# Kernel tuning notes

Measured on AMD Instinct MI355X. Metric: run time of the kernel, lower is better.

The kernel has to match this reference:

```python
import jax, jax.numpy as jnp
import numpy as np

EMBED = 1024
HEADS = 16
HEAD_DIM = EMBED // HEADS


def setup_inputs() -> dict:
    key = jax.random.key(0)
    ks = jax.random.split(key, 11)
    B, S, D = 4, 2048, EMBED
    scale = 1.0 / np.sqrt(D)
    inp = {
        "query": jax.random.normal(ks[0], (B, S, D), dtype=jnp.float32),
        "key": jax.random.normal(ks[1], (B, S, D), dtype=jnp.float32),
        "value": jax.random.normal(ks[2], (B, S, D), dtype=jnp.float32),
        "Wq": jax.random.normal(ks[3], (D, D), dtype=jnp.float32) * scale,
        "bq": jnp.zeros((D,), dtype=jnp.float32),
        "Wk": jax.random.normal(ks[4], (D, D), dtype=jnp.float32) * scale,
        "bk": jnp.zeros((D,), dtype=jnp.float32),
        "Wv": jax.random.normal(ks[5], (D, D), dtype=jnp.float32) * scale,
        "bv": jnp.zeros((D,), dtype=jnp.float32),
        "Wo": jax.random.normal(ks[6], (D, D), dtype=jnp.float32) * scale,
        "bo": jnp.zeros((D,), dtype=jnp.float32),
    }
    return inp


def reference(query, key, value, Wq, bq, Wk, bk, Wv, bv, Wo, bo):
    B, S, D = query.shape
    H, Hd = HEADS, HEAD_DIM

    def split_heads(x):  # [B,S,D] -> [B,H,S,Hd]
        return x.reshape(B, -1, H, Hd).transpose(0, 2, 1, 3)

    q = split_heads(query @ Wq.T + bq)
    k = split_heads(key @ Wk.T + bk)
    v = split_heads(value @ Wv.T + bv)
    # [B,H,S,S] scores (explicitly materialized, as in the original)
    attn = jnp.einsum("bhsd,bhtd->bhst", q, k) / jnp.sqrt(jnp.float32(Hd))
    attn = jax.nn.softmax(attn, axis=-1)  # dropout p=0.0 is identity
    out = jnp.einsum("bhst,bhtd->bhsd", attn, v)
    out = out.transpose(0, 2, 1, 3).reshape(B, -1, D)
    return out @ Wo.T + bo
```

## Files before the change

kernel.cpp:

```cpp
#include <hip/hip_runtime.h>
#include <stdint.h>

typedef __bf16 bf16x8_t __attribute__((ext_vector_type(8)));
typedef float f32x2_t __attribute__((ext_vector_type(2)));
typedef float f32x4_t __attribute__((ext_vector_type(4)));
typedef float f32x8_t __attribute__((ext_vector_type(8)));
typedef float f32x16_t __attribute__((ext_vector_type(16)));
typedef uint16_t u16x8_t __attribute__((ext_vector_type(8)));
typedef uint16_t u16x4_t __attribute__((ext_vector_type(4)));
typedef uint32_t u32x4_t __attribute__((ext_vector_type(4)));

#define MFMA16(a, b, c) __builtin_amdgcn_mfma_f32_16x16x32_bf16((a), (b), (c), 0, 0, 0)
#define MFMA32(a, b, c) __builtin_amdgcn_mfma_f32_32x32x16_bf16((a), (b), (c), 0, 0, 0)

__device__ __forceinline__ void gll16(const void* g, void* l) {
  typedef const __attribute__((address_space(1))) void* gp1_t;
  typedef __attribute__((address_space(3))) void* lp3_t;
  __builtin_amdgcn_global_load_lds((gp1_t)(uintptr_t)g,
                                   (lp3_t)(uint32_t)(uintptr_t)l, 16, 0, 0);
}

__device__ __forceinline__ uint16_t f2bf(float f) {
  uint32_t u = __float_as_uint(f);
  u += 0x7fffu + ((u >> 16) & 1u);
  return (uint16_t)(u >> 16);
}

__device__ __forceinline__ uint32_t cvtpk(float lo, float hi) {
  uint32_t r;
  asm("v_cvt_pk_bf16_f32 %0, %1, %2" : "=v"(r) : "v"(lo), "v"(hi));
  return r;
}

__device__ __forceinline__ void pl32swap(uint32_t& x, uint32_t& y) {
  asm("v_permlane32_swap_b32 %0, %1" : "+v"(x), "+v"(y));
}

__device__ __forceinline__ float fexp2(float x) {
#if __has_builtin(__builtin_amdgcn_exp2f)
  return __builtin_amdgcn_exp2f(x);
#else
  return exp2f(x);
#endif
}

__global__ __launch_bounds__(256) void cvt_all_kernel(
    const float* __restrict__ q, const float* __restrict__ k, const float* __restrict__ v,
    const float* __restrict__ wq, const float* __restrict__ wk, const float* __restrict__ wv,
    const float* __restrict__ wo, uint16_t* __restrict__ oq, uint16_t* __restrict__ ok,
    uint16_t* __restrict__ ov, uint16_t* __restrict__ owq, uint16_t* __restrict__ owk,
    uint16_t* __restrict__ owv, uint16_t* __restrict__ owo, float qscale) {
  const int bid = blockIdx.x;
  const float* in;
  uint16_t* out;
  int i;
  float sc = 1.0f;
  if (bid < 12288) {
    const int seg = bid >> 12;
    in = seg == 0 ? q : (seg == 1 ? k : v);
    out = seg == 0 ? oq : (seg == 1 ? ok : ov);
    i = (bid & 4095) * 256 + threadIdx.x;
  } else {
    const int wb = bid - 12288, seg = wb >> 9;
    in = seg == 0 ? wq : (seg == 1 ? wk : (seg == 2 ? wv : wo));
    out = seg == 0 ? owq : (seg == 1 ? owk : (seg == 2 ? owv : owo));
    if (seg == 0) sc = qscale;
    i = (wb & 511) * 256 + threadIdx.x;
  }
  const float4* p = (const float4*)in;
  float4 a = p[2 * i], b = p[2 * i + 1];
  u16x8_t o;
  o[0] = f2bf(a.x * sc); o[1] = f2bf(a.y * sc);
  o[2] = f2bf(a.z * sc); o[3] = f2bf(a.w * sc);
  o[4] = f2bf(b.x * sc); o[5] = f2bf(b.y * sc);
  o[6] = f2bf(b.z * sc); o[7] = f2bf(b.w * sc);
  ((u16x8_t*)out)[i] = o;
}

#define GEMM_KLOOP(Ab, Bb)                                                                   \
  _Pragma("unroll") for (int s = 0; s < 4; ++s) {                                            \
    const int rbase = s * 32 + w * 8;                                                        \
    gll16(Ab + (size_t)(bm0 + rbase + srow) * (K * 2) + scb, AsB + rbase * 128);             \
    gll16(Bb + (size_t)(bn0 + rbase + srow) * (K * 2) + scb, BsB + rbase * 128);             \
  }                                                                                          \
  for (int it = 0; it < K / 64; ++it) {                                                      \
    const int cur = (it & 1) * 16384;                                                        \
    asm volatile("s_waitcnt vmcnt(0)\ns_barrier" ::: "memory");                              \
    if (it < 15) {                                                                           \
      const int k0 = (it + 1) * 64;                                                          \
      const int nxt = (cur ^ 16384);                                                         \
      _Pragma("unroll") for (int s = 0; s < 4; ++s) {                                        \
        const int rbase = s * 32 + w * 8;                                                    \
        gll16(Ab + (size_t)(bm0 + rbase + srow) * (K * 2) + k0 * 2 + scb,                    \
              AsB + nxt + rbase * 128);                                                      \
        gll16(Bb + (size_t)(bn0 + rbase + srow) * (K * 2) + k0 * 2 + scb,                    \
              BsB + nxt + rbase * 128);                                                      \
      }                                                                                      \
    }                                                                                        \
    _Pragma("unroll") for (int kk = 0; kk < 2; ++kk) {                                       \
      bf16x8_t af[4], bfr[4];                                                                \
      _Pragma("unroll") for (int f = 0; f < 4; ++f) {                                        \
        const int ar = wr * 64 + f * 16 + lrow;                                              \
        af[f] =                                                                              \
            *(const bf16x8_t*)(AsB + cur + ar * 128 + ((kk * 64 + g * 16) ^ ((ar & 7) << 4)));\
        const int br = wc * 64 + f * 16 + lrow;                                              \
        bfr[f] =                                                                             \
            *(const bf16x8_t*)(BsB + cur + br * 128 + ((kk * 64 + g * 16) ^ ((br & 7) << 4)));\
      }                                                                                      \
      __builtin_amdgcn_s_setprio(1);                                                         \
      _Pragma("unroll") for (int fm = 0; fm < 4; ++fm) _Pragma("unroll")                     \
          for (int fn = 0; fn < 4; ++fn) acc[fm][fn] = MFMA16(af[fm], bfr[fn], acc[fm][fn]); \
      __builtin_amdgcn_s_setprio(0);                                                         \
    }                                                                                        \
  }

__global__ __launch_bounds__(256) void gemm_qkv_kernel(
    const uint16_t* __restrict__ Xq, const uint16_t* __restrict__ Xk,
    const uint16_t* __restrict__ Xv, const uint16_t* __restrict__ Wqb,
    const uint16_t* __restrict__ Wkb, const uint16_t* __restrict__ Wvb,
    const float* __restrict__ bq, const float* __restrict__ bk, const float* __restrict__ bv,
    uint16_t* __restrict__ Qp, uint16_t* __restrict__ Kp, uint16_t* __restrict__ VTp,
    float qscale) {
  constexpr int K = 1024, N = 1024;
  __shared__ uint16_t As[2][128 * 64];
  __shared__ uint16_t Bs[2][128 * 64];
  char* AsB = (char*)As;
  char* BsB = (char*)Bs;
  const int tid = threadIdx.x;
  const int w = tid >> 6, l = tid & 63;
  const int wr = w >> 1, wc = w & 1;
  const int lrow = l & 15, g = l >> 4;
  const int bm0 = blockIdx.y * 128, bn0 = blockIdx.x * 128;
  const int srow = l >> 3;
  const int scb = ((l & 7) ^ srow) << 4;
  const int z = blockIdx.z;
  const char* Ab = (const char*)(z == 0 ? Xq : (z == 1 ? Xk : Xv));
  const char* Bb = (const char*)(z == 0 ? Wqb : (z == 1 ? Wkb : Wvb));
  const float* bias = z == 0 ? bq : (z == 1 ? bk : bv);
  const float alpha = z == 0 ? qscale : 1.0f;
  f32x4_t acc[4][4] = {};

  GEMM_KLOOP(Ab, Bb)

#pragma unroll
  for (int fn = 0; fn < 4; ++fn) {
    const int col = bn0 + wc * 64 + fn * 16 + lrow;
    const float bv_ = bias[col] * alpha;
#pragma unroll
    for (int fm = 0; fm < 4; ++fm) {
      const int row0 = bm0 + wr * 64 + fm * 16 + g * 4;
      const int b = row0 >> 11, t = row0 & 2047;
      const int bhh = (b << 4) + (col >> 6), d = col & 63;
      if (z == 0) {
#pragma unroll
        for (int r = 0; r < 4; ++r)
          Qp[(size_t)(row0 + r) * N + col] = f2bf(acc[fm][fn][r] + bv_);
      } else if (z == 1) {
#pragma unroll
        for (int r = 0; r < 4; ++r)
          Kp[((size_t)bhh * 2048 + t + r) * 64 + d] = f2bf(acc[fm][fn][r] + bv_);
      } else {
        u16x4_t pv;
#pragma unroll
        for (int r = 0; r < 4; ++r) pv[r] = f2bf(acc[fm][fn][r] + bv_);
        const size_t idx = (((size_t)bhh * 32 + (t >> 6)) * 64 + d) * 64 + (t & 63);
        *(u16x4_t*)(VTp + idx) = pv;
      }
    }
  }
}

__global__ __launch_bounds__(256) void gemm_out_kernel(const uint16_t* __restrict__ A,
                                                       const uint16_t* __restrict__ Bw,
                                                       const float* __restrict__ bias,
                                                       float* __restrict__ C) {
  constexpr int K = 1024, N = 1024;
  __shared__ uint16_t As[2][128 * 64];
  __shared__ uint16_t Bs[2][128 * 64];
  char* AsB = (char*)As;
  char* BsB = (char*)Bs;
  const int tid = threadIdx.x;
  const int w = tid >> 6, l = tid & 63;
  const int wr = w >> 1, wc = w & 1;
  const int lrow = l & 15, g = l >> 4;
  const int bm0 = blockIdx.y * 128, bn0 = blockIdx.x * 128;
  const int srow = l >> 3;
  const int scb = ((l & 7) ^ srow) << 4;
  const char* Ab = (const char*)A;
  const char* Bb = (const char*)Bw;
  f32x4_t acc[4][4] = {};

  GEMM_KLOOP(Ab, Bb)

#pragma unroll
  for (int fn = 0; fn < 4; ++fn) {
    const int col = bn0 + wc * 64 + fn * 16 + lrow;
    const float bv_ = bias[col];
#pragma unroll
    for (int fm = 0; fm < 4; ++fm) {
      const int row0 = bm0 + wr * 64 + fm * 16 + g * 4;
#pragma unroll
      for (int r = 0; r < 4; ++r) C[(size_t)(row0 + r) * N + col] = acc[fm][fn][r] + bv_;
    }
  }
}

__global__ __launch_bounds__(256, 4) void attn_kernel(const uint16_t* __restrict__ Q,
                                                      const uint16_t* __restrict__ Kh,
                                                      const uint16_t* __restrict__ VT,
                                                      uint16_t* __restrict__ AO) {
  constexpr int S = 2048, D = 1024;
  __shared__ uint16_t Kb[2][64 * 64];
  __shared__ uint16_t Vb[2][64 * 64];
  char* KbB = (char*)Kb;
  char* VbB = (char*)Vb;
  const int tid = threadIdx.x;
  const int w = tid >> 6, l = tid & 63;
  const int lr = l & 31, hi = l >> 5;
  const int flat = blockIdx.x;
  const int xcd = flat & 7, ii = flat >> 3;
  const int bh = xcd * 8 + (ii & 7);
  const int qt = ii >> 3;
  const int b = bh >> 4, h = bh & 15;
  const int q0 = qt * 128;
  const int srow = l >> 3;
  const int sofs0 = (w * 8 + srow) * 128 + (((l & 7) ^ srow ^ (w & 3)) << 4);
  const int swz = ((l & 7) ^ ((l >> 3) & 3)) << 4;
  const char* Kg = (const char*)Kh + (size_t)bh * 262144;
  const char* Vg = (const char*)VT + (size_t)bh * 262144;

  const char* qrow =
      (const char*)Q + (size_t)(b * S + q0 + w * 32 + lr) * (D * 2) + h * 128 + hi * 16;
  bf16x8_t qf[4];
#pragma unroll
  for (int km = 0; km < 4; ++km) qf[km] = *(const bf16x8_t*)(qrow + km * 32);

  float l_run = 0.f;
  f32x16_t acco[2] = {};

  gll16(Kg + sofs0, KbB + w * 1024);
  gll16(Kg + 4096 + sofs0, KbB + 4096 + w * 1024);
  gll16(Vg + sofs0, VbB + w * 1024);
  gll16(Vg + 4096 + sofs0, VbB + 4096 + w * 1024);

#pragma unroll 2
  for (int t = 0; t < 32; ++t) {
    const int cur = (t & 1) * 8192;
    asm volatile("s_waitcnt vmcnt(0)\ns_barrier" ::: "memory");

    if (t < 31) {
      const size_t nb = (size_t)(t + 1) * 8192 + sofs0;
      const int nl = (cur ^ 8192) + w * 1024;
      gll16(Kg + nb, KbB + nl);
      gll16(Kg + nb + 4096, KbB + nl + 4096);
      gll16(Vg + nb, VbB + nl);
      gll16(Vg + nb + 4096, VbB + nl + 4096);
    }

    f32x16_t s0 = {}, s1 = {};
    __builtin_amdgcn_s_setprio(1);
#pragma unroll
    for (int km = 0; km < 4; ++km) {
      const int co = (km * 32 + hi * 16) ^ swz;
      bf16x8_t kf0 = *(const bf16x8_t*)(KbB + cur + lr * 128 + co);
      bf16x8_t kf1 = *(const bf16x8_t*)(KbB + cur + (32 + lr) * 128 + co);
      s0 = MFMA32(kf0, qf[km], s0);
      s1 = MFMA32(kf1, qf[km], s1);
    }
    __builtin_amdgcn_s_setprio(0);

#pragma unroll
    for (int j = 0; j < 16; ++j) {
      s0[j] = fexp2(s0[j]);
      s1[j] = fexp2(s1[j]);
    }
    {
      f32x16_t sv = s0 + s1;
      f32x8_t a8 = __builtin_shufflevector(sv, sv, 0, 1, 2, 3, 4, 5, 6, 7) +
                   __builtin_shufflevector(sv, sv, 8, 9, 10, 11, 12, 13, 14, 15);
      f32x4_t a4 = __builtin_shufflevector(a8, a8, 0, 1, 2, 3) +
                   __builtin_shufflevector(a8, a8, 4, 5, 6, 7);
      f32x2_t a2 = __builtin_shufflevector(a4, a4, 0, 1) +
                   __builtin_shufflevector(a4, a4, 2, 3);
      float rs = a2[0] + a2[1];
      rs += __shfl_xor(rs, 32);
      l_run += rs;
    }

    uint32_t cw[16];
#pragma unroll
    for (int j = 0; j < 8; ++j) cw[j] = cvtpk(s0[2 * j], s0[2 * j + 1]);
#pragma unroll
    for (int j = 0; j < 8; ++j) cw[8 + j] = cvtpk(s1[2 * j], s1[2 * j + 1]);
    pl32swap(cw[0], cw[2]);
    pl32swap(cw[1], cw[3]);
    pl32swap(cw[4], cw[6]);
    pl32swap(cw[5], cw[7]);
    pl32swap(cw[8], cw[10]);
    pl32swap(cw[9], cw[11]);
    pl32swap(cw[12], cw[14]);
    pl32swap(cw[13], cw[15]);

    __builtin_amdgcn_s_setprio(1);
#pragma unroll
    for (int kb = 0; kb < 4; ++kb) {
      u32x4_t pwv = {cw[kb * 4], cw[kb * 4 + 1], cw[kb * 4 + 2], cw[kb * 4 + 3]};
      bf16x8_t pa = __builtin_bit_cast(bf16x8_t, pwv);
#pragma unroll
      for (int db = 0; db < 2; ++db) {
        bf16x8_t vf = *(const bf16x8_t*)(VbB + cur + (db * 32 + lr) * 128 +
                                         ((kb * 32 + hi * 16) ^ swz));
        acco[db] = MFMA32(vf, pa, acco[db]);
      }
    }
    __builtin_amdgcn_s_setprio(0);
  }

  const float inv = 1.0f / l_run;
  uint16_t* orow = AO + (size_t)(b * S + q0 + w * 32 + lr) * D + h * 64 + hi * 4;
#pragma unroll
  for (int db = 0; db < 2; ++db)
#pragma unroll
    for (int rr = 0; rr < 4; ++rr) {
      u16x4_t o;
#pragma unroll
      for (int j = 0; j < 4; ++j) o[j] = f2bf(acco[db][rr * 4 + j] * inv);
      *(u16x4_t*)(orow + db * 32 + rr * 8) = o;
    }
}

extern "C" void kernel_launch(void* const* d_in, const int* in_sizes, int n_in,
                              void* d_out, int out_size, void* d_ws, size_t ws_size,
                              hipStream_t stream) {
  const float* q_in = (const float*)d_in[0];
  const float* k_in = (const float*)d_in[1];
  const float* v_in = (const float*)d_in[2];
  const float* Wq = (const float*)d_in[3];
  const float* bq = (const float*)d_in[4];
  const float* Wk = (const float*)d_in[5];
  const float* bk = (const float*)d_in[6];
  const float* Wv = (const float*)d_in[7];
  const float* bv = (const float*)d_in[8];
  const float* Wo = (const float*)d_in[9];
  const float* bo = (const float*)d_in[10];

  const size_t MD = (size_t)8192 * 1024;
  const size_t DD = (size_t)1024 * 1024;
  uint16_t* Xq = (uint16_t*)d_ws;
  uint16_t* Xk = Xq + MD;
  uint16_t* Xv = Xk + MD;
  uint16_t* Wqb = Xv + MD;
  uint16_t* Wkb = Wqb + DD;
  uint16_t* Wvb = Wkb + DD;
  uint16_t* Wob = Wvb + DD;
  uint16_t* Qp = Wob + DD;
  uint16_t* Kp = Qp + MD;
  uint16_t* VTp = Kp + MD;
  uint16_t* AO = Xq;

  const float QSCALE = 0.125f * 1.44269504088896f;

  cvt_all_kernel<<<14336, 256, 0, stream>>>(q_in, k_in, v_in, Wq, Wk, Wv, Wo, Xq, Xk, Xv,
                                            Wqb, Wkb, Wvb, Wob, QSCALE);

  gemm_qkv_kernel<<<dim3(8, 64, 3), 256, 0, stream>>>(Xq, Xk, Xv, Wqb, Wkb, Wvb, bq, bk, bv,
                                                      Qp, Kp, VTp, QSCALE);

  attn_kernel<<<1024, 256, 0, stream>>>(Qp, Kp, VTp, AO);

  gemm_out_kernel<<<dim3(8, 64), 256, 0, stream>>>(AO, Wob, bo, (float*)d_out);
}
```

Measured before the change: 199.8 us.

## Fuse fp32-to-bf16 activation conversion into QKV GEMM A-tile loading

The separate conversion pass over the q/k/v activations is removed. The QKV GEMM now loads fp32 A tiles into registers, converts them to bf16 with packed converts, and writes them into swizzled LDS for the next stage, while the weights still stream through global_load_lds. This avoids writing and re-reading 48MB of bf16 intermediates, at the cost of the GEMM reading each fp32 A tile 8 times (once per N-block), using more registers, and using a simpler register-staged pipeline. The attention kernel also moves the cross-lane row-sum shuffle out of the inner loop to a single shuffle at the end.

Measured after the change: 228.3 us, median of 3. 1.14x slower.

```diff
diff --git a/kernel.cpp b/kernel.cpp
--- a/kernel.cpp
+++ b/kernel.cpp
@@ -44,29 +44,16 @@
 #endif
 }
 
-__global__ __launch_bounds__(256) void cvt_all_kernel(
-    const float* __restrict__ q, const float* __restrict__ k, const float* __restrict__ v,
+__global__ __launch_bounds__(256) void cvt_w_kernel(
     const float* __restrict__ wq, const float* __restrict__ wk, const float* __restrict__ wv,
-    const float* __restrict__ wo, uint16_t* __restrict__ oq, uint16_t* __restrict__ ok,
-    uint16_t* __restrict__ ov, uint16_t* __restrict__ owq, uint16_t* __restrict__ owk,
+    const float* __restrict__ wo, uint16_t* __restrict__ owq, uint16_t* __restrict__ owk,
     uint16_t* __restrict__ owv, uint16_t* __restrict__ owo, float qscale) {
   const int bid = blockIdx.x;
-  const float* in;
-  uint16_t* out;
-  int i;
-  float sc = 1.0f;
-  if (bid < 12288) {
-    const int seg = bid >> 12;
-    in = seg == 0 ? q : (seg == 1 ? k : v);
-    out = seg == 0 ? oq : (seg == 1 ? ok : ov);
-    i = (bid & 4095) * 256 + threadIdx.x;
-  } else {
-    const int wb = bid - 12288, seg = wb >> 9;
-    in = seg == 0 ? wq : (seg == 1 ? wk : (seg == 2 ? wv : wo));
-    out = seg == 0 ? owq : (seg == 1 ? owk : (seg == 2 ? owv : owo));
-    if (seg == 0) sc = qscale;
-    i = (wb & 511) * 256 + threadIdx.x;
-  }
+  const int seg = bid >> 9;
+  const float* in = seg == 0 ? wq : (seg == 1 ? wk : (seg == 2 ? wv : wo));
+  uint16_t* out = seg == 0 ? owq : (seg == 1 ? owk : (seg == 2 ? owv : owo));
+  const float sc = seg == 0 ? qscale : 1.0f;
+  const int i = (bid & 511) * 256 + threadIdx.x;
   const float4* p = (const float4*)in;
   float4 a = p[2 * i], b = p[2 * i + 1];
   u16x8_t o;
@@ -115,8 +102,8 @@
   }
 
 __global__ __launch_bounds__(256) void gemm_qkv_kernel(
-    const uint16_t* __restrict__ Xq, const uint16_t* __restrict__ Xk,
-    const uint16_t* __restrict__ Xv, const uint16_t* __restrict__ Wqb,
+    const float* __restrict__ Xq32, const float* __restrict__ Xk32,
+    const float* __restrict__ Xv32, const uint16_t* __restrict__ Wqb,
     const uint16_t* __restrict__ Wkb, const uint16_t* __restrict__ Wvb,
     const float* __restrict__ bq, const float* __restrict__ bk, const float* __restrict__ bv,
     uint16_t* __restrict__ Qp, uint16_t* __restrict__ Kp, uint16_t* __restrict__ VTp,
@@ -133,14 +120,77 @@
   const int bm0 = blockIdx.y * 128, bn0 = blockIdx.x * 128;
   const int srow = l >> 3;
   const int scb = ((l & 7) ^ srow) << 4;
+  const int acol = ((l & 7) ^ srow) * 8;
   const int z = blockIdx.z;
-  const char* Ab = (const char*)(z == 0 ? Xq : (z == 1 ? Xk : Xv));
+  const float* A32 = z == 0 ? Xq32 : (z == 1 ? Xk32 : Xv32);
   const char* Bb = (const char*)(z == 0 ? Wqb : (z == 1 ? Wkb : Wvb));
   const float* bias = z == 0 ? bq : (z == 1 ? bk : bv);
   const float alpha = z == 0 ? qscale : 1.0f;
   f32x4_t acc[4][4] = {};
-
-  GEMM_KLOOP(Ab, Bb)
+  float4 ar0[4], ar1[4];
+
+#define QKV_A_LOAD(k0)                                                             \
+  _Pragma("unroll") for (int s = 0; s < 4; ++s) {                                  \
+    const int rbase = s * 32 + w * 8;                                              \
+    const float* ap = A32 + (size_t)(bm0 + rbase + srow) * 1024 + (k0) + acol;     \
+    ar0[s] = *(const float4*)ap;                                                   \
+    ar1[s] = *(const float4*)(ap + 4);                                             \
+  }
+#define QKV_B_STAGE(k0, dst)                                                       \
+  _Pragma("unroll") for (int s = 0; s < 4; ++s) {                                  \
+    const int rbase = s * 32 + w * 8;                                              \
+    gll16(Bb + (size_t)(bn0 + rbase + srow) * (K * 2) + (k0) * 2 + scb,            \
+          BsB + (dst) + rbase * 128);                                              \
+  }
+#define QKV_A_WRITE(dst)                                                           \
+  _Pragma("unroll") for (int s = 0; s < 4; ++s) {                                  \
+    const int rbase = s * 32 + w * 8;                                              \
+    u32x4_t wv = {cvtpk(ar0[s].x, ar0[s].y), cvtpk(ar0[s].z, ar0[s].w),            \
+                  cvtpk(ar1[s].x, ar1[s].y), cvtpk(ar1[s].z, ar1[s].w)};           \
+    *(u32x4_t*)(AsB + (dst) + rbase * 128 + l * 16) = wv;                          \
+  }
+
+  QKV_A_LOAD(0)
+  QKV_B_STAGE(0, 0)
+  QKV_A_WRITE(0)
+
+  for (int it = 0; it < K / 64; ++it) {
+    const int cur = (it & 1) * 16384;
+    asm volatile("s_waitcnt vmcnt(0) lgkmcnt(0)\ns_barrier" ::: "memory");
+
+    const int nxt = cur ^ 16384;
+    if (it < 15) {
+      const int k0 = (it + 1) * 64;
+      QKV_A_LOAD(k0)
+      QKV_B_STAGE(k0, nxt)
+    }
+
+#pragma unroll
+    for (int kk = 0; kk < 2; ++kk) {
+      bf16x8_t af[4], bfr[4];
+#pragma unroll
+      for (int f = 0; f < 4; ++f) {
+        const int ar = wr * 64 + f * 16 + lrow;
+        af[f] = *(const bf16x8_t*)(AsB + cur + ar * 128 + ((kk * 64 + g * 16) ^ ((ar & 7) << 4)));
+        const int br = wc * 64 + f * 16 + lrow;
+        bfr[f] = *(const bf16x8_t*)(BsB + cur + br * 128 + ((kk * 64 + g * 16) ^ ((br & 7) << 4)));
+      }
+      __builtin_amdgcn_s_setprio(1);
+#pragma unroll
+      for (int fm = 0; fm < 4; ++fm)
+#pragma unroll
+        for (int fn = 0; fn < 4; ++fn)
+          acc[fm][fn] = MFMA16(af[fm], bfr[fn], acc[fm][fn]);
+      __builtin_amdgcn_s_setprio(0);
+    }
+
+    if (it < 15) {
+      QKV_A_WRITE(nxt)
+    }
+  }
+#undef QKV_A_LOAD
+#undef QKV_B_STAGE
+#undef QKV_A_WRITE
 
 #pragma unroll
   for (int fn = 0; fn < 4; ++fn) {
@@ -282,9 +332,7 @@
                    __builtin_shufflevector(a8, a8, 4, 5, 6, 7);
       f32x2_t a2 = __builtin_shufflevector(a4, a4, 0, 1) +
                    __builtin_shufflevector(a4, a4, 2, 3);
-      float rs = a2[0] + a2[1];
-      rs += __shfl_xor(rs, 32);
-      l_run += rs;
+      l_run += a2[0] + a2[1];
     }
 
     uint32_t cw[16];
@@ -316,6 +364,7 @@
     __builtin_amdgcn_s_setprio(0);
   }
 
+  l_run += __shfl_xor(l_run, 32);
   const float inv = 1.0f / l_run;
   uint16_t* orow = AO + (size_t)(b * S + q0 + w * 32 + lr) * D + h * 64 + hi * 4;
 #pragma unroll
@@ -346,25 +395,21 @@
 
   const size_t MD = (size_t)8192 * 1024;
   const size_t DD = (size_t)1024 * 1024;
-  uint16_t* Xq = (uint16_t*)d_ws;
-  uint16_t* Xk = Xq + MD;
-  uint16_t* Xv = Xk + MD;
-  uint16_t* Wqb = Xv + MD;
+  uint16_t* AO = (uint16_t*)d_ws;
+  uint16_t* Wqb = AO + 3 * MD;
   uint16_t* Wkb = Wqb + DD;
   uint16_t* Wvb = Wkb + DD;
   uint16_t* Wob = Wvb + DD;
   uint16_t* Qp = Wob + DD;
   uint16_t* Kp = Qp + MD;
   uint16_t* VTp = Kp + MD;
-  uint16_t* AO = Xq;
 
   const float QSCALE = 0.125f * 1.44269504088896f;
 
-  cvt_all_kernel<<<14336, 256, 0, stream>>>(q_in, k_in, v_in, Wq, Wk, Wv, Wo, Xq, Xk, Xv,
-                                            Wqb, Wkb, Wvb, Wob, QSCALE);
-
-  gemm_qkv_kernel<<<dim3(8, 64, 3), 256, 0, stream>>>(Xq, Xk, Xv, Wqb, Wkb, Wvb, bq, bk, bv,
-                                                      Qp, Kp, VTp, QSCALE);
+  cvt_w_kernel<<<2048, 256, 0, stream>>>(Wq, Wk, Wv, Wo, Wqb, Wkb, Wvb, Wob, QSCALE);
+
+  gemm_qkv_kernel<<<dim3(8, 64, 3), 256, 0, stream>>>(q_in, k_in, v_in, Wqb, Wkb, Wvb,
+                                                      bq, bk, bv, Qp, Kp, VTp, QSCALE);
 
   attn_kernel<<<1024, 256, 0, stream>>>(Qp, Kp, VTp, AO);
 
```
